# Kernel tuning notes

Measured on AMD Instinct MI355X. Metric: run time of the kernel, lower is better.

The kernel has to match this reference:

```python
import jax, jax.numpy as jnp
import numpy as np

N_QUBITS = 12
N_LAYERS = 6
BATCH = 8192
D_IN = 512


def _apply_1q(state, gate, wire):
    # state: [B] + [2]*n (real), gate: [2,2]. new[j] = sum_i gate[j,i]*old[i]
    s = jnp.moveaxis(state, 1 + wire, -1)
    s = jnp.einsum('...i,ji->...j', s, gate)
    return jnp.moveaxis(s, -1, 1 + wire)


def _apply_cnot(state, ctrl, tgt):
    # flip target amplitude pair where control bit == 1
    s = jnp.moveaxis(state, (1 + ctrl, 1 + tgt), (-2, -1))
    s = jnp.concatenate([s[..., :1, :], s[..., 1:, ::-1]], axis=-2)
    return jnp.moveaxis(s, (-2, -1), (1 + ctrl, 1 + tgt))


def _simulate(angles, weights):
    # angles: [B, n] per-sample RY angles; weights: [L, n] shared RY angles.
    # Circuit: H + RY(angle) per wire on |0>, then L x (RY layer + CNOT chain).
    # All gates are real -> real float32 statevector.
    B, n = angles.shape
    L = weights.shape[0]
    inv_sqrt2 = jnp.float32(1.0 / np.sqrt(2.0))
    half = 0.5 * angles
    c, s = jnp.cos(half), jnp.sin(half)
    # per-wire single-qubit state RY(a) @ H @ |0> = inv_sqrt2 * [c-s, c+s]
    v = inv_sqrt2 * jnp.stack([c - s, c + s], axis=-1)  # [B, n, 2]
    state = v[:, 0]  # [B, 2]
    for w in range(1, n):
        state = jnp.einsum('b...,bj->b...j', state, v[:, w])  # product state
    # state: [B] + [2]*n
    for layer in range(L):
        h = 0.5 * weights[layer]
        cl, sl = jnp.cos(h), jnp.sin(h)
        for w in range(n):
            gate = jnp.stack([jnp.stack([cl[w], -sl[w]]),
                              jnp.stack([sl[w], cl[w]])])
            state = _apply_1q(state, gate, w)
        for w in range(n - 1):
            state = _apply_cnot(state, w, w + 1)
    probs = state * state
    zs = []
    for w in range(n):
        axes = tuple(a for a in range(1, n + 1) if a != 1 + w)
        p = probs.sum(axis=axes)  # [B, 2]
        zs.append(p[:, 0] - p[:, 1])
    return jnp.stack(zs, axis=-1)  # [B, n] = <Z_i>


def setup_inputs() -> dict:
    key = jax.random.key(0)
    ks = jax.random.split(key, 6)
    x = jax.random.normal(ks[0], (BATCH, D_IN), jnp.float32)
    pre_w = jax.random.normal(ks[1], (N_QUBITS, D_IN), jnp.float32) / np.sqrt(D_IN)
    pre_b = jax.random.normal(ks[2], (N_QUBITS,), jnp.float32) * 0.01
    weights = jax.random.normal(ks[3], (N_LAYERS, N_QUBITS), jnp.float32)
    post_w = jax.random.normal(ks[4], (1, N_QUBITS), jnp.float32) / np.sqrt(N_QUBITS)
    post_b = jax.random.normal(ks[5], (1,), jnp.float32) * 0.01
    return {"x": x, "pre_w": pre_w, "pre_b": pre_b, "weights": weights,
            "post_w": post_w, "post_b": post_b}


def reference(x, pre_w, pre_b, weights, post_w, post_b):
    pre = x @ pre_w.T + pre_b                # [B, n_qubits]
    angles = pre * jnp.float32(np.pi / 2.0)  # RY(inputs[i]*pi/2)
    q_out = _simulate(angles, weights)       # [B, n_qubits]
    return q_out @ post_w.T + post_b         # [B, 1]
```

## Files before the change

kernel.cpp:

```cpp
#include <hip/hip_runtime.h>
#include <math.h>

#define NQ 12
#define NL 6
#define BATCHN 8192
#define DIN 512

typedef _Float16 f16;
typedef __attribute__((ext_vector_type(8)))  _Float16 f16x8;
typedef __attribute__((ext_vector_type(16))) float    f32x16;
typedef unsigned int u32;
typedef __attribute__((ext_vector_type(4))) u32 u32x4;
typedef __attribute__((ext_vector_type(2))) int i32x2;


__device__ __forceinline__ u32 pkrtz(float a, float b) {
  auto p = __builtin_amdgcn_cvt_pkrtz(a, b);
  return __builtin_bit_cast(u32, p);
}
__device__ __forceinline__ u32 bperm(int addr, u32 v) {
  return (u32)__builtin_amdgcn_ds_bpermute(addr, (int)v);
}
__device__ __forceinline__ float dppx1(float v) {
  return __int_as_float(__builtin_amdgcn_mov_dpp(__float_as_int(v), 0xB1, 0xF, 0xF, true));
}
__device__ __forceinline__ u32 dppx1u(u32 v) {
  return (u32)__builtin_amdgcn_mov_dpp((int)v, 0xB1, 0xF, 0xF, true);
}
__device__ __forceinline__ float dppx2(float v) {
  return __int_as_float(__builtin_amdgcn_mov_dpp(__float_as_int(v), 0x4E, 0xF, 0xF, true));
}
__device__ __forceinline__ float dppx8(float v) {
  return __int_as_float(__builtin_amdgcn_mov_dpp(__float_as_int(v), 0x128, 0xF, 0xF, true));
}
template <int PAT>
__device__ __forceinline__ float swzf(float v) {
  return __int_as_float(__builtin_amdgcn_ds_swizzle(__float_as_int(v), PAT));
}

#if __has_builtin(__builtin_amdgcn_permlane32_swap)
__device__ __forceinline__ void pswap(u32& a, u32& b) {
  i32x2 r = __builtin_amdgcn_permlane32_swap((int)a, (int)b, false, false);
  a = (u32)r.x; b = (u32)r.y;
}
#else
#define PSWAP_FALLBACK 1
__device__ __forceinline__ void pswap_fb(u32& a, u32& b, bool hi, int axor) {
  u32 xa = bperm(axor, a), xb = bperm(axor, b);
  u32 na = hi ? xb : a;
  u32 nb = hi ? b : xa;
  a = na; b = nb;
}
#endif

__device__ __forceinline__ float wave_sum(float v) {
  v += dppx1(v);
  v += dppx2(v);
  v += swzf<0x101F>(v);
  v += dppx8(v);
  v += swzf<0x401F>(v);
#ifndef PSWAP_FALLBACK
  u32 a = __builtin_bit_cast(u32, v), b = a;
  pswap(a, b);
  return __builtin_bit_cast(float, a) + __builtin_bit_cast(float, b);
#else
  return v + __shfl_xor(v, 32, 64);
#endif
}
__device__ __forceinline__ f16x8 asf(const u32 a[4]) {
  u32x4 v; v.x = a[0]; v.y = a[1]; v.z = a[2]; v.w = a[3];
  return __builtin_bit_cast(f16x8, v);
}
__device__ __forceinline__ f16x8 ldB(const u32* __restrict__ p, int off) {
  u32x4 v = *(const u32x4*)(p + off);
  return __builtin_bit_cast(f16x8, v);
}

#if __has_builtin(__builtin_amdgcn_global_load_lds)
#define HAVE_GLLDS 1
__device__ __forceinline__ void stage_mat(const u32* __restrict__ Bg,
                                          u32* lbuf, int wid, int lane) {
  #pragma unroll
  for (int c2 = 0; c2 < 2; ++c2) {
    const int c = wid * 2 + c2;
    const u32* g = Bg + c * 256 + lane * 4;
    u32* l = lbuf + c * 256;
    __builtin_amdgcn_global_load_lds(
        (const __attribute__((address_space(1))) u32*)g,
        (__attribute__((address_space(3))) u32*)l, 16, 0, 0);
  }
}
#else
__device__ __forceinline__ void stage_mat(const u32* __restrict__ Bg,
                                          u32* lbuf, int wid, int lane) {
  #pragma unroll
  for (int c2 = 0; c2 < 2; ++c2) {
    const int c = wid * 2 + c2;
    u32x4 v = *(const u32x4*)(Bg + c * 256 + lane * 4);
    *(u32x4*)(lbuf + c * 256 + lane * 4) = v;
  }
}
#endif

__device__ __forceinline__ void sincos_rev(float rev, float* s, float* c) {
  float r = rev - floorf(rev);
#if __has_builtin(__builtin_amdgcn_sinf) && __has_builtin(__builtin_amdgcn_cosf)
  *s = __builtin_amdgcn_sinf(r);
  *c = __builtin_amdgcn_cosf(r);
#else
  const float TWO_PI = 6.28318530717958647693f;
  sincosf(r * TWO_PI, s, c);
#endif
}

__device__ __forceinline__ u32 foldw(u32 w, u32 m) {
  u32 partner = dppx1u(w);
  return (m & partner) | (~m & w);
}

__global__ void setup_mats(const float* __restrict__ weights, u32* __restrict__ Bbuf) {
  const int mm = blockIdx.x >> 3;
  const int l  = mm >> 1;
  const int qs = mm & 1;
  __shared__ float c6[6], s6[6];
  if (threadIdx.x < 6) {
    float h = 0.5f * weights[l * NQ + qs * 6 + threadIdx.x];
    c6[threadIdx.x] = cosf(h);
    s6[threadIdx.x] = sinf(h);
  }
  __syncthreads();
  const int t = (blockIdx.x & 7) * 256 + threadIdx.x;
  const int lane = (t >> 2) & 63;
  const int fk   = t >> 8;
  const int kt   = fk & 3;
  const int nt   = fk >> 2;
  const int n     = nt * 32 + (lane & 31);
  const int kbase = kt * 16 + (lane >> 5) * 8 + (t & 3) * 2;
  float v[2];
  #pragma unroll
  for (int u = 0; u < 2; ++u) {
    int k = kbase + u;
    int bb = k;
    if (l >= 1) { bb ^= bb << 1; bb ^= bb << 2; bb ^= bb << 4; bb &= 63; }
    float prod = 1.f;
    #pragma unroll
    for (int w = 0; w < 6; ++w) {
      const int aw = (n >> w) & 1, bw = (bb >> w) & 1;
      prod *= (aw == bw) ? c6[w] : (aw ? s6[w] : -s6[w]);
    }
    v[u] = prod;
  }
  Bbuf[mm * 2048 + t] = pkrtz(v[0], v[1]);
}

template <bool FOLD>
__device__ __forceinline__ void mm_step(f32x16 (&d)[2][2],
                                        const u32* Bl,
                                        u32 maskA, u32 maskB) {
  f16x8 Bc0 = ldB(Bl, 0 * 256);
  f16x8 Bc1 = ldB(Bl, 4 * 256);
  u32 fr[2][4][4];
  #pragma unroll
  for (int kt = 0; kt < 4; ++kt) {
    const int s  = kt >> 1;
    const int b0 = 4 * ((2 * kt) & 3);
    const int b1 = 4 * ((2 * kt + 1) & 3);
    #pragma unroll
    for (int mt = 0; mt < 2; ++mt) {
      u32 p0a = pkrtz(d[s][mt][b0 + 0], d[s][mt][b0 + 1]);
      u32 p0b = pkrtz(d[s][mt][b0 + 2], d[s][mt][b0 + 3]);
      u32 p1a = pkrtz(d[s][mt][b1 + 0], d[s][mt][b1 + 1]);
      u32 p1b = pkrtz(d[s][mt][b1 + 2], d[s][mt][b1 + 3]);
      if (FOLD) {
        const int PAR4[4] = {0, 1, 1, 0};
        const int ka = (PAR4[b0 >> 2] + s) & 1;
        const int kc = (PAR4[b1 >> 2] + s) & 1;
        p0a = foldw(p0a, ka ? maskB : maskA);
        p0b = foldw(p0b, ka ? maskA : maskB);
        p1a = foldw(p1a, kc ? maskB : maskA);
        p1b = foldw(p1b, kc ? maskA : maskB);
      }
#ifdef PSWAP_FALLBACK
      pswap_fb(p0a, p1a, false, 0);
      pswap_fb(p0b, p1b, false, 0);
#else
      pswap(p0a, p1a);
      pswap(p0b, p1b);
#endif
      fr[mt][kt][0] = p0a;
      fr[mt][kt][1] = p0b;
      fr[mt][kt][2] = p1a;
      fr[mt][kt][3] = p1b;
    }
  }
  #pragma unroll
  for (int kt = 0; kt < 4; ++kt) {
    f16x8 B0 = Bc0, B1 = Bc1;
    if (kt < 3) {
      Bc0 = ldB(Bl, (kt + 1) * 256);
      Bc1 = ldB(Bl, (4 + kt + 1) * 256);
    }
    f16x8 A0 = asf(fr[0][kt]);
    f16x8 A1 = asf(fr[1][kt]);
    if (kt == 0) {
      f32x16 z{};
      d[0][0] = __builtin_amdgcn_mfma_f32_32x32x16_f16(A0, B0, z, 0, 0, 0);
      d[0][1] = __builtin_amdgcn_mfma_f32_32x32x16_f16(A0, B1, z, 0, 0, 0);
      d[1][0] = __builtin_amdgcn_mfma_f32_32x32x16_f16(A1, B0, z, 0, 0, 0);
      d[1][1] = __builtin_amdgcn_mfma_f32_32x32x16_f16(A1, B1, z, 0, 0, 0);
    } else {
      d[0][0] = __builtin_amdgcn_mfma_f32_32x32x16_f16(A0, B0, d[0][0], 0, 0, 0);
      d[0][1] = __builtin_amdgcn_mfma_f32_32x32x16_f16(A0, B1, d[0][1], 0, 0, 0);
      d[1][0] = __builtin_amdgcn_mfma_f32_32x32x16_f16(A1, B0, d[1][0], 0, 0, 0);
      d[1][1] = __builtin_amdgcn_mfma_f32_32x32x16_f16(A1, B1, d[1][1], 0, 0, 0);
    }
  }
}

__global__ void __launch_bounds__(256) __attribute__((amdgpu_waves_per_eu(3, 4)))
dqc_main(const float* __restrict__ x,
         const float* __restrict__ pre_w,
         const float* __restrict__ pre_b,
         const float* __restrict__ weights,
         const float* __restrict__ post_w,
         const float* __restrict__ post_b,
         const u32* __restrict__ Bbuf,
         float* __restrict__ out)
{
  const int lane = threadIdx.x & 63;
  const int wid  = threadIdx.x >> 6;
  const bool hi  = lane >= 32;
  const int b    = blockIdx.x * 4 + wid;
  const u32 maskA = hi ? 0x0000FFFFu : 0xFFFF0000u;
  const u32 maskB = ~maskA;

  __shared__ __align__(16) u32 Bs[2][2048];
  stage_mat(Bbuf + 2 * 2048, &Bs[0][0], wid, lane);
  stage_mat(Bbuf + 3 * 2048, &Bs[1][0], wid, lane);

  float acc[NQ];
  const float* xr = x + (size_t)b * DIN + lane * 8;
  const float4 xa = *(const float4*)(xr);
  const float4 xb = *(const float4*)(xr + 4);
  #pragma unroll
  for (int w = 0; w < NQ; ++w) {
    const float* wr = pre_w + w * DIN + lane * 8;
    const float4 wa = *(const float4*)(wr);
    const float4 wb = *(const float4*)(wr + 4);
    acc[w] = xa.x * wa.x + xa.y * wa.y + xa.z * wa.z + xa.w * wa.w
           + xb.x * wb.x + xb.y * wb.y + xb.z * wb.z + xb.w * wb.w;
  }
  #pragma unroll
  for (int w = 0; w < NQ; ++w) acc[w] = wave_sum(acc[w]);

  const float INV_4PI = 0.07957747154594766788f;
  float u0[NQ], u1[NQ];
  #pragma unroll
  for (int w = 0; w < NQ; ++w) {
    const float cw2 = 0.125f + pre_b[w] * 0.125f + weights[w] * INV_4PI;
    const float rev = fmaf(acc[w], 0.125f, cw2);
    sincos_rev(rev, &u1[w], &u0[w]);
  }

  float base8[8];
  #pragma unroll
  for (int j = 0; j < 8; ++j)
    base8[j] = ((j & 1) ? u1[0] : u0[0]) * ((j & 2) ? u1[1] : u0[1]) * ((j & 4) ? u1[2] : u0[2]);
  float hiP[4];
  #pragma unroll
  for (int kt = 0; kt < 4; ++kt)
    hiP[kt] = (hi ? u1[3] : u0[3]) * ((kt & 1) ? u1[4] : u0[4]) * ((kt & 2) ? u1[5] : u0[5]);
  const float q5 = ((lane & 2) ? u1[7] : u0[7]) * ((lane & 4) ? u1[8] : u0[8])
                 * ((lane & 8) ? u1[9] : u0[9]) * ((lane & 16) ? u1[10] : u0[10]);
  const float qA = q5 * ((lane & 1) ? u1[6] : u0[6]);
  const float qB = q5 * ((lane & 1) ? u0[6] : u1[6]);
  const float qeven = hi ? qB : qA;
  const float qodd  = hi ? qA : qB;
  const float qe0 = qeven * u0[11], qo0 = qodd * u0[11];
  const float qe1 = qeven * u1[11], qo1 = qodd * u1[11];

  asm volatile("s_waitcnt vmcnt(0)" ::: "memory");
  __syncthreads();

  const u32* B0p = &Bs[0][0] + lane * 4;
  const u32* B1p = &Bs[1][0] + lane * 4;

  f32x16 d[2][2];
  {
    f16x8 Ic0 = ldB(B0p, 0 * 256);
    f16x8 Ic1 = ldB(B0p, 4 * 256);
    const int PKT[4] = {0, 1, 1, 0};
    const int PDW[4] = {0, 1, 1, 0};
    #pragma unroll
    for (int kt = 0; kt < 4; ++kt) {
      u32 a0[4], a1[4];
      #pragma unroll
      for (int dw = 0; dw < 4; ++dw) {
        const float e0 = base8[2 * dw] * hiP[kt];
        const float e1 = base8[2 * dw + 1] * hiP[kt];
        const bool cls = (PKT[kt] ^ PDW[dw]) != 0;
        a0[dw] = pkrtz((cls ? qo0 : qe0) * e0, (cls ? qe0 : qo0) * e1);
        a1[dw] = pkrtz((cls ? qo1 : qe1) * e0, (cls ? qe1 : qo1) * e1);
      }
      f16x8 B0 = Ic0, B1 = Ic1;
      if (kt < 3) {
        Ic0 = ldB(B0p, (kt + 1) * 256);
        Ic1 = ldB(B0p, (4 + kt + 1) * 256);
      }
      f16x8 A0 = asf(a0), A1 = asf(a1);
      if (kt == 0) {
        f32x16 z{};
        d[0][0] = __builtin_amdgcn_mfma_f32_32x32x16_f16(A0, B0, z, 0, 0, 0);
        d[0][1] = __builtin_amdgcn_mfma_f32_32x32x16_f16(A0, B1, z, 0, 0, 0);
        d[1][0] = __builtin_amdgcn_mfma_f32_32x32x16_f16(A1, B0, z, 0, 0, 0);
        d[1][1] = __builtin_amdgcn_mfma_f32_32x32x16_f16(A1, B1, z, 0, 0, 0);
      } else {
        d[0][0] = __builtin_amdgcn_mfma_f32_32x32x16_f16(A0, B0, d[0][0], 0, 0, 0);
        d[0][1] = __builtin_amdgcn_mfma_f32_32x32x16_f16(A0, B1, d[0][1], 0, 0, 0);
        d[1][0] = __builtin_amdgcn_mfma_f32_32x32x16_f16(A1, B0, d[1][0], 0, 0, 0);
        d[1][1] = __builtin_amdgcn_mfma_f32_32x32x16_f16(A1, B1, d[1][1], 0, 0, 0);
      }
    }
  }

  #define STEP_TAIL(nextmm, bufidx)                                  \
    do {                                                             \
      asm volatile("s_waitcnt vmcnt(0)" ::: "memory");               \
      __syncthreads();                                               \
      stage_mat(Bbuf + (nextmm) * 2048, &Bs[bufidx][0], wid, lane);  \
    } while (0)

  STEP_TAIL(4, 0);
  mm_step<false>(d, B1p, maskA, maskB);
  STEP_TAIL(5, 1);
  mm_step<true >(d, B0p, maskA, maskB);
  STEP_TAIL(6, 0);
  mm_step<false>(d, B1p, maskA, maskB);
  STEP_TAIL(7, 1);
  mm_step<true >(d, B0p, maskA, maskB);
  STEP_TAIL(8, 0);
  mm_step<false>(d, B1p, maskA, maskB);
  STEP_TAIL(9, 1);
  mm_step<true >(d, B0p, maskA, maskB);
  STEP_TAIL(10, 0);
  mm_step<false>(d, B1p, maskA, maskB);
  STEP_TAIL(11, 1);
  mm_step<true >(d, B0p, maskA, maskB);
  asm volatile("s_waitcnt vmcnt(0)" ::: "memory");
  __syncthreads();
  mm_step<false>(d, B1p, maskA, maskB);
  #undef STEP_TAIL

  const float pw0 = post_w[0], pw1 = post_w[1], pw2 = post_w[2],
              pw3 = post_w[3], pw4 = post_w[4], pw5 = post_w[5];
  float A0s = 0.f, A1s = 0.f, s00 = 0.f, s01 = 0.f, accA = 0.f, accB = 0.f;
  #pragma unroll
  for (int mt = 0; mt < 2; ++mt)
    #pragma unroll
    for (int nt = 0; nt < 2; ++nt)
      #pragma unroll
      for (int r = 0; r < 16; ++r) {
        float v = d[mt][nt][r];
        float sq = v * v;
        const int par0 = (__builtin_popcount(r & 3) + __builtin_popcount(r >> 2) + mt) & 1;
        if (par0) A1s += sq; else A0s += sq;
        if (nt == 0) { if (par0) s01 += sq; else s00 += sq; }
        const int c0 = r & 1;
        const int c1 = (r ^ (r >> 1)) & 1;
        const int c3 = c1 ^ ((r >> 2) & 1);
        const int c4 = c3 ^ ((r >> 3) & 1);
        const int c5 = c4 ^ mt;
        const float ca = (c0 ? -pw0 : pw0) + (c1 ? -pw1 : pw1);
        const float cb = (c1 ? -pw2 : pw2) + (c3 ? -pw3 : pw3)
                       + (c4 ? -pw4 : pw4) + (c5 ? -pw5 : pw5);
        accA = fmaf(ca, sq, accA);
        accB = fmaf(cb, sq, accB);
      }
  const float sgnhi = hi ? -1.f : 1.f;
  const float tot   = A0s + A1s;
  const float diff  = sgnhi * (A0s - A1s);
  const float diffs = sgnhi * (2.f * (s00 - s01) - (A0s - A1s));
  float Sq = 0.f;
  #pragma unroll
  for (int j = 0; j < 5; ++j) {
    const int par = __builtin_popcount(lane & ((2 << j) - 1)) & 1;
    Sq += par ? -post_w[6 + j] : post_w[6 + j];
  }
  const float s5 = (__builtin_popcount(lane & 31) & 1) ? -post_w[11] : post_w[11];
  const float zcomb = accA + sgnhi * accB + diff * Sq + diffs * s5;

  const float tots = wave_sum(tot);
  const float zs   = wave_sum(zcomb);

  if (lane == 0) {
    out[b] = fmaf(zs, 1.0f / tots, post_b[0]);
  }
}

extern "C" void kernel_launch(void* const* d_in, const int* in_sizes, int n_in,
                              void* d_out, int out_size, void* d_ws, size_t ws_size,
                              hipStream_t stream) {
  (void)in_sizes; (void)n_in; (void)out_size; (void)ws_size;
  const float* x       = (const float*)d_in[0];
  const float* pre_w   = (const float*)d_in[1];
  const float* pre_b   = (const float*)d_in[2];
  const float* weights = (const float*)d_in[3];
  const float* post_w  = (const float*)d_in[4];
  const float* post_b  = (const float*)d_in[5];
  float* out = (float*)d_out;
  u32* Bbuf = (u32*)d_ws;

  setup_mats<<<96, 256, 0, stream>>>(weights, Bbuf);
  dqc_main<<<BATCHN / 4, 256, 0, stream>>>(x, pre_w, pre_b, weights,
                                           post_w, post_b, Bbuf, out);
}
```

Before: 116.1 us.

## Quad-buffer LDS matrix staging to halve barriers, raise MFMA wave priority

Grows the shared-memory staging area from two to four 8 KB matrix buffers and stages two matrices per barrier, so the ten remaining mm_steps need about half as many s_waitcnt+__syncthreads points. It also wraps the MFMA loop in mm_step with s_setprio(1)/s_setprio(0) so matrix issue is favoured over other waves. The cost is doubled LDS per block (32 KB), which may limit how many blocks fit per CU. Each barrier now waits for two in-flight global-to-LDS loads at once.

Result: no change. 115.5 us (-0.6%).

```diff
diff --git a/kernel.cpp b/kernel.cpp
--- a/kernel.cpp
+++ b/kernel.cpp
@@ -18,9 +18,6 @@
   auto p = __builtin_amdgcn_cvt_pkrtz(a, b);
   return __builtin_bit_cast(u32, p);
 }
-__device__ __forceinline__ u32 bperm(int addr, u32 v) {
-  return (u32)__builtin_amdgcn_ds_bpermute(addr, (int)v);
-}
 __device__ __forceinline__ float dppx1(float v) {
   return __int_as_float(__builtin_amdgcn_mov_dpp(__float_as_int(v), 0xB1, 0xF, 0xF, true));
 }
@@ -46,7 +43,8 @@
 #else
 #define PSWAP_FALLBACK 1
 __device__ __forceinline__ void pswap_fb(u32& a, u32& b, bool hi, int axor) {
-  u32 xa = bperm(axor, a), xb = bperm(axor, b);
+  u32 xa = (u32)__builtin_amdgcn_ds_bpermute(axor, (int)a);
+  u32 xb = (u32)__builtin_amdgcn_ds_bpermute(axor, (int)b);
   u32 na = hi ? xb : a;
   u32 nb = hi ? b : xa;
   a = na; b = nb;
@@ -71,13 +69,12 @@
   u32x4 v; v.x = a[0]; v.y = a[1]; v.z = a[2]; v.w = a[3];
   return __builtin_bit_cast(f16x8, v);
 }
-__device__ __forceinline__ f16x8 ldB(const u32* __restrict__ p, int off) {
+__device__ __forceinline__ f16x8 ldB(const u32* p, int off) {
   u32x4 v = *(const u32x4*)(p + off);
   return __builtin_bit_cast(f16x8, v);
 }
 
 #if __has_builtin(__builtin_amdgcn_global_load_lds)
-#define HAVE_GLLDS 1
 __device__ __forceinline__ void stage_mat(const u32* __restrict__ Bg,
                                           u32* lbuf, int wid, int lane) {
   #pragma unroll
@@ -193,6 +190,7 @@
       fr[mt][kt][3] = p1b;
     }
   }
+  __builtin_amdgcn_s_setprio(1);
   #pragma unroll
   for (int kt = 0; kt < 4; ++kt) {
     f16x8 B0 = Bc0, B1 = Bc1;
@@ -215,6 +213,7 @@
       d[1][1] = __builtin_amdgcn_mfma_f32_32x32x16_f16(A1, B1, d[1][1], 0, 0, 0);
     }
   }
+  __builtin_amdgcn_s_setprio(0);
 }
 
 __global__ void __launch_bounds__(256) __attribute__((amdgpu_waves_per_eu(3, 4)))
@@ -234,9 +233,11 @@
   const u32 maskA = hi ? 0x0000FFFFu : 0xFFFF0000u;
   const u32 maskB = ~maskA;
 
-  __shared__ __align__(16) u32 Bs[2][2048];
+  __shared__ __align__(16) u32 Bs[4][2048];
   stage_mat(Bbuf + 2 * 2048, &Bs[0][0], wid, lane);
   stage_mat(Bbuf + 3 * 2048, &Bs[1][0], wid, lane);
+  stage_mat(Bbuf + 4 * 2048, &Bs[2][0], wid, lane);
+  stage_mat(Bbuf + 5 * 2048, &Bs[3][0], wid, lane);
 
   float acc[NQ];
   const float* xr = x + (size_t)b * DIN + lane * 8;
@@ -282,13 +283,15 @@
   asm volatile("s_waitcnt vmcnt(0)" ::: "memory");
   __syncthreads();
 
-  const u32* B0p = &Bs[0][0] + lane * 4;
-  const u32* B1p = &Bs[1][0] + lane * 4;
+  const u32* Bp0 = &Bs[0][0] + lane * 4;
+  const u32* Bp1 = &Bs[1][0] + lane * 4;
+  const u32* Bp2 = &Bs[2][0] + lane * 4;
+  const u32* Bp3 = &Bs[3][0] + lane * 4;
 
   f32x16 d[2][2];
   {
-    f16x8 Ic0 = ldB(B0p, 0 * 256);
-    f16x8 Ic1 = ldB(B0p, 4 * 256);
+    f16x8 Ic0 = ldB(Bp0, 0 * 256);
+    f16x8 Ic1 = ldB(Bp0, 4 * 256);
     const int PKT[4] = {0, 1, 1, 0};
     const int PDW[4] = {0, 1, 1, 0};
     #pragma unroll
@@ -304,8 +307,8 @@
       }
       f16x8 B0 = Ic0, B1 = Ic1;
       if (kt < 3) {
-        Ic0 = ldB(B0p, (kt + 1) * 256);
-        Ic1 = ldB(B0p, (4 + kt + 1) * 256);
+        Ic0 = ldB(Bp0, (kt + 1) * 256);
+        Ic1 = ldB(Bp0, (4 + kt + 1) * 256);
       }
       f16x8 A0 = asf(a0), A1 = asf(a1);
       if (kt == 0) {
@@ -323,33 +326,29 @@
     }
   }
 
-  #define STEP_TAIL(nextmm, bufidx)                                  \
-    do {                                                             \
-      asm volatile("s_waitcnt vmcnt(0)" ::: "memory");               \
-      __syncthreads();                                               \
-      stage_mat(Bbuf + (nextmm) * 2048, &Bs[bufidx][0], wid, lane);  \
+  #define BAR_STAGE2(mmA, bufA, mmB, bufB)                            \
+    do {                                                              \
+      asm volatile("s_waitcnt vmcnt(0)" ::: "memory");                \
+      __syncthreads();                                                \
+      stage_mat(Bbuf + (mmA) * 2048, &Bs[bufA][0], wid, lane);        \
+      stage_mat(Bbuf + (mmB) * 2048, &Bs[bufB][0], wid, lane);        \
     } while (0)
 
-  STEP_TAIL(4, 0);
-  mm_step<false>(d, B1p, maskA, maskB);
-  STEP_TAIL(5, 1);
-  mm_step<true >(d, B0p, maskA, maskB);
-  STEP_TAIL(6, 0);
-  mm_step<false>(d, B1p, maskA, maskB);
-  STEP_TAIL(7, 1);
-  mm_step<true >(d, B0p, maskA, maskB);
-  STEP_TAIL(8, 0);
-  mm_step<false>(d, B1p, maskA, maskB);
-  STEP_TAIL(9, 1);
-  mm_step<true >(d, B0p, maskA, maskB);
-  STEP_TAIL(10, 0);
-  mm_step<false>(d, B1p, maskA, maskB);
-  STEP_TAIL(11, 1);
-  mm_step<true >(d, B0p, maskA, maskB);
+  mm_step<false>(d, Bp1, maskA, maskB);
+  BAR_STAGE2(6, 0, 7, 1);
+  mm_step<true >(d, Bp2, maskA, maskB);
+  mm_step<false>(d, Bp3, maskA, maskB);
+  BAR_STAGE2(8, 2, 9, 3);
+  mm_step<true >(d, Bp0, maskA, maskB);
+  mm_step<false>(d, Bp1, maskA, maskB);
+  BAR_STAGE2(10, 0, 11, 1);
+  mm_step<true >(d, Bp2, maskA, maskB);
+  mm_step<false>(d, Bp3, maskA, maskB);
   asm volatile("s_waitcnt vmcnt(0)" ::: "memory");
   __syncthreads();
-  mm_step<false>(d, B1p, maskA, maskB);
-  #undef STEP_TAIL
+  mm_step<true >(d, Bp0, maskA, maskB);
+  mm_step<false>(d, Bp1, maskA, maskB);
+  #undef BAR_STAGE2
 
   const float pw0 = post_w[0], pw1 = post_w[1], pw2 = post_w[2],
               pw3 = post_w[3], pw4 = post_w[4], pw5 = post_w[5];
```
